# Kernel tuning notes

Measured on AMD Instinct MI355X. Metric: run time of the kernel, lower is better.

Reference implementation:

```python
import jax, jax.numpy as jnp
import numpy as np

DD = 1.5        # delta_d margin from config (paper default)
GAMMA = 0.001   # regularization weight from config (paper default)
K = 32          # number of instance ids (fixed num_segments; labels in [0, K))


def _per_image_loss(feats, labels):
    """feats: (D, H, W) float, labels: (H, W) int. Returns scalar loss."""
    D = feats.shape[0]
    f = feats.reshape(D, -1).T              # (N, D) pixel embeddings
    lab = labels.reshape(-1)                # (N,)

    counts = jax.ops.segment_sum(jnp.ones(lab.shape, f.dtype), lab, num_segments=K)  # (K,)
    present = counts > 0
    safe_cnt = jnp.maximum(counts, 1.0)

    sums = jax.ops.segment_sum(f, lab, num_segments=K)      # (K, D)
    means = sums / safe_cnt[:, None]                        # (K, D)

    # variance term: sum_i ||f_i - mu_{lab_i}||^2, per-instance-normalized
    d2 = jnp.sum((f - means[lab]) ** 2, axis=1)             # (N,)
    var_per = jax.ops.segment_sum(d2, lab, num_segments=K) / safe_cnt
    var_loss = jnp.sum(jnp.where(present, var_per, 0.0))

    # pairwise distance (hinge) term over i < j, only present clusters
    diff = means[:, None, :] - means[None, :, :]            # (K, K, D)
    dsq = jnp.sum(diff ** 2, axis=-1)                       # (K, K)
    pair_mask = jnp.triu(jnp.ones((K, K), bool), 1) & present[:, None] & present[None, :]
    dist = jnp.sqrt(jnp.where(pair_mask, dsq, 1.0))
    hinge = jnp.where(pair_mask & (dist < 2.0 * DD), (2.0 * DD - dist) ** 2, 0.0)
    n_clusters = jnp.sum(present).astype(f.dtype)
    dist_loss = jnp.sum(hinge) / jnp.maximum(n_clusters - 1.0, 1.0)

    # regularization: sum of L2 norms of present means
    m2 = jnp.sum(means ** 2, axis=1)
    reg_loss = jnp.sum(jnp.where(present, jnp.sqrt(jnp.where(present, m2, 1.0)), 0.0))

    return (var_loss + dist_loss + GAMMA * reg_loss) / n_clusters


def setup_inputs() -> dict:
    key = jax.random.key(0)
    k1, k2 = jax.random.split(key)
    B, D, H, W = 4, 64, 512, 512
    features_batch = jax.random.normal(k1, (B, D, H, W), dtype=jnp.float32)
    labels_batch = jax.random.randint(k2, (B, H, W), 0, K, dtype=jnp.int32)
    return {"features_batch": features_batch, "labels_batch": labels_batch}


def reference(features_batch, labels_batch):
    per_image = jax.vmap(_per_image_loss)(features_batch, labels_batch)  # (B,)
    B = features_batch.shape[0]
    return (jnp.sum(per_image) / (B + 1)).reshape(1)
```

## Files before the change

### kernel.cpp

```cpp
#include <hip/hip_runtime.h>
#include <hip/hip_bf16.h>
#include <math.h>


#define KSEG 32
#define DF   64
#define STATS_STRIDE 2112
#define GPB  512

typedef _Float16 half8 __attribute__((ext_vector_type(8)));
typedef float f32x4 __attribute__((ext_vector_type(4)));

__global__ __launch_bounds__(256) void stats_kernel(
    const float* __restrict__ feats, const int* __restrict__ labels,
    float* __restrict__ st, int N) {
  const int b = blockIdx.y, g = blockIdx.x;
  const int tid = threadIdx.x;
  const int w = tid >> 6, lane = tid & 63;
  const int m = lane & 15, q = lane >> 4;

  const float* __restrict__ fimg = feats + (size_t)b * DF * N;
  const int* __restrict__ limg = labels + (size_t)b * N;
  const int pix0 = g * (N / GPB);
  const int d = 16 * w + m;
  const float* __restrict__ frow = fimg + (size_t)d * N;

  f32x4 c_sum0 = {0.f, 0.f, 0.f, 0.f}, c_sum1 = {0.f, 0.f, 0.f, 0.f};
  f32x4 c_sq0 = {0.f, 0.f, 0.f, 0.f}, c_sq1 = {0.f, 0.f, 0.f, 0.f};
  f32x4 c_cn0 = {0.f, 0.f, 0.f, 0.f}, c_cn1 = {0.f, 0.f, 0.f, 0.f};
  const _Float16 h1 = (_Float16)1.0f, h0 = (_Float16)0.0f;
  half8 ones = {h1, h1, h1, h1, h1, h1, h1, h1};

#pragma unroll 4
  for (int c = 0; c < 16; ++c) {
    const int pb = pix0 + c * 32 + q * 8;
    const float4 fA = *(const float4*)(frow + pb);
    const float4 fB = *(const float4*)(frow + pb + 4);
    const int4 lA = *(const int4*)(limg + pb);
    const int4 lB = *(const int4*)(limg + pb + 4);

    float fv[8] = {fA.x, fA.y, fA.z, fA.w, fB.x, fB.y, fB.z, fB.w};
    int lv[8] = {lA.x, lA.y, lA.z, lA.w, lB.x, lB.y, lB.z, lB.w};

    half8 bf, bsq, a0, a1;
#pragma unroll
    for (int j = 0; j < 8; ++j) {
      const _Float16 h = (_Float16)fv[j];
      bf[j] = h;
      bsq[j] = h * h;
      a0[j] = (lv[j] == m) ? h1 : h0;
      a1[j] = (lv[j] == m + 16) ? h1 : h0;
    }
    c_sum0 = __builtin_amdgcn_mfma_f32_16x16x32_f16(a0, bf, c_sum0, 0, 0, 0);
    c_sum1 = __builtin_amdgcn_mfma_f32_16x16x32_f16(a1, bf, c_sum1, 0, 0, 0);
    c_sq0 = __builtin_amdgcn_mfma_f32_16x16x32_f16(a0, bsq, c_sq0, 0, 0, 0);
    c_sq1 = __builtin_amdgcn_mfma_f32_16x16x32_f16(a1, bsq, c_sq1, 0, 0, 0);
    c_cn0 = __builtin_amdgcn_mfma_f32_16x16x32_f16(a0, ones, c_cn0, 0, 0, 0);
    c_cn1 = __builtin_amdgcn_mfma_f32_16x16x32_f16(a1, ones, c_cn1, 0, 0, 0);
  }

  __shared__ float lsum[KSEG][DF + 1];
  __shared__ float lssq[KSEG][DF + 1];
  __shared__ float lcnt[KSEG];
#pragma unroll
  for (int r = 0; r < 4; ++r) {
    const int k0 = q * 4 + r;
    lsum[k0][16 * w + m] = c_sum0[r];
    lsum[k0 + 16][16 * w + m] = c_sum1[r];
    lssq[k0][16 * w + m] = c_sq0[r];
    lssq[k0 + 16][16 * w + m] = c_sq1[r];
  }
  if (w == 0 && m == 0) {
#pragma unroll
    for (int r = 0; r < 4; ++r) {
      lcnt[q * 4 + r] = c_cn0[r];
      lcnt[16 + q * 4 + r] = c_cn1[r];
    }
  }
  __syncthreads();

  float* so = st + (size_t)b * STATS_STRIDE;
  for (int i = tid; i < KSEG * DF; i += 256)
    atomicAdd(&so[i], lsum[i >> 6][i & 63]);
  if (tid < KSEG) {
    float s = 0.f;
    for (int dd = 0; dd < DF; ++dd) s += lssq[tid][dd];
    atomicAdd(&so[KSEG * DF + tid], lcnt[tid]);
    atomicAdd(&so[KSEG * DF + KSEG + tid], s);
  }
}

__global__ __launch_bounds__(256) void finalize_kernel(
    const float* __restrict__ st, float* __restrict__ out, int B) {
  __shared__ float mu[KSEG][DF + 1];
  __shared__ float cntS[KSEG], ssqS[KSEG], musqS[KSEG];
  __shared__ float wred[4];
  const int tid = threadIdx.x;
  float total = 0.f;

  for (int b = 0; b < B; ++b) {
    const float* base = st + (size_t)b * STATS_STRIDE;
    if (tid < KSEG) {
      cntS[tid] = base[KSEG * DF + tid];
      ssqS[tid] = base[KSEG * DF + KSEG + tid];
    }
    __syncthreads();
    for (int idx = tid; idx < KSEG * DF; idx += 256) {
      const int k = idx >> 6, dd = idx & 63;
      mu[k][dd] = base[idx] / fmaxf(cntS[k], 1.f);
    }
    __syncthreads();
    if (tid < KSEG) {
      float m2 = 0.f;
      for (int dd = 0; dd < DF; ++dd) m2 = fmaf(mu[tid][dd], mu[tid][dd], m2);
      musqS[tid] = m2;
    }
    __syncthreads();

    float hacc = 0.f;
    for (int p = tid; p < KSEG * KSEG; p += 256) {
      const int i = p >> 5, j = p & 31;
      if (i < j && cntS[i] > 0.f && cntS[j] > 0.f) {
        float dsq = 0.f;
        for (int dd = 0; dd < DF; ++dd) {
          const float df = mu[i][dd] - mu[j][dd];
          dsq = fmaf(df, df, dsq);
        }
        const float h = 2.f * 1.5f - sqrtf(dsq);
        if (h > 0.f) hacc += h * h;
      }
    }
    for (int off = 32; off > 0; off >>= 1) hacc += __shfl_down(hacc, off, 64);
    if ((tid & 63) == 0) wred[tid >> 6] = hacc;
    __syncthreads();

    if (tid == 0) {
      const float dsum = wred[0] + wred[1] + wred[2] + wred[3];
      float var = 0.f, reg = 0.f, ncl = 0.f;
      for (int k = 0; k < KSEG; ++k) {
        const float c = cntS[k];
        if (c > 0.f) {
          ncl += 1.f;
          var += ssqS[k] / c - musqS[k];
          reg += sqrtf(musqS[k]);
        }
      }
      const float dist_loss = dsum / fmaxf(ncl - 1.f, 1.f);
      total += (var + dist_loss + 0.001f * reg) / ncl;
    }
    __syncthreads();
  }
  if (tid == 0) out[0] = total / (float)(B + 1);
}

extern "C" void kernel_launch(void* const* d_in, const int* in_sizes, int n_in,
                              void* d_out, int out_size, void* d_ws, size_t ws_size,
                              hipStream_t stream) {
  const float* feats = (const float*)d_in[0];
  const int* labels = (const int*)d_in[1];
  float* out = (float*)d_out;

  const int B = 4;
  const int BHW = in_sizes[1];
  const int N = BHW / B;

  float* st = (float*)d_ws;
  hipMemsetAsync(st, 0, (size_t)B * STATS_STRIDE * sizeof(float), stream);

  stats_kernel<<<dim3(GPB, B), 256, 0, stream>>>(feats, labels, st, N);
  finalize_kernel<<<1, 256, 0, stream>>>(st, out, B);
}
```

Measured before the change: 419.8 us.

## Replace global atomics with per-block partials and a two-stage tree reduction

Each stats block now writes its per-segment partial sums to its own workspace slot instead of atomically adding into one shared buffer per image. A new reduce kernel sums the partials in 16 groups, and finalize runs one block per image, adding its loss into the output with an atomic. This removes heavy atomic contention (about 2K atomics from each of 2048 blocks onto the same addresses) and the memset, at the cost of roughly 17 MB of extra partial traffic and an extra kernel launch. Zeroing the output inside reduce_kernel relies on stream ordering before finalize.

After: 398.9 us. 5.0% less time.

```diff
diff --git a/kernel.cpp b/kernel.cpp
--- a/kernel.cpp
+++ b/kernel.cpp
@@ -1,5 +1,4 @@
 #include <hip/hip_runtime.h>
-#include <hip/hip_bf16.h>
 #include <math.h>
 
 
@@ -7,13 +6,15 @@
 #define DF   64
 #define STATS_STRIDE 2112
 #define GPB  512
+#define ZSPLIT 16
+#define GPZ  (GPB / ZSPLIT)
 
 typedef _Float16 half8 __attribute__((ext_vector_type(8)));
 typedef float f32x4 __attribute__((ext_vector_type(4)));
 
 __global__ __launch_bounds__(256) void stats_kernel(
     const float* __restrict__ feats, const int* __restrict__ labels,
-    float* __restrict__ st, int N) {
+    float* __restrict__ partial, int N) {
   const int b = blockIdx.y, g = blockIdx.x;
   const int tid = threadIdx.x;
   const int w = tid >> 6, lane = tid & 63;
@@ -79,78 +80,97 @@
   }
   __syncthreads();
 
-  float* so = st + (size_t)b * STATS_STRIDE;
+  float* so = partial + (size_t)(b * GPB + g) * STATS_STRIDE;
   for (int i = tid; i < KSEG * DF; i += 256)
-    atomicAdd(&so[i], lsum[i >> 6][i & 63]);
+    so[i] = lsum[i >> 6][i & 63];
   if (tid < KSEG) {
     float s = 0.f;
     for (int dd = 0; dd < DF; ++dd) s += lssq[tid][dd];
-    atomicAdd(&so[KSEG * DF + tid], lcnt[tid]);
-    atomicAdd(&so[KSEG * DF + KSEG + tid], s);
+    so[KSEG * DF + tid] = lcnt[tid];
+    so[KSEG * DF + KSEG + tid] = s;
   }
 }
 
+__global__ __launch_bounds__(256) void reduce_kernel(
+    const float* __restrict__ partial, float* __restrict__ p2,
+    float* __restrict__ out) {
+  if (blockIdx.x == 0 && blockIdx.y == 0 && blockIdx.z == 0 && threadIdx.x == 0)
+    out[0] = 0.f;
+  const int idx = blockIdx.x * 256 + threadIdx.x;
+  if (idx >= STATS_STRIDE) return;
+  const int b = blockIdx.y, z = blockIdx.z;
+  const float* __restrict__ src =
+      partial + (size_t)(b * GPB + z * GPZ) * STATS_STRIDE + idx;
+  float s = 0.f;
+#pragma unroll 8
+  for (int g = 0; g < GPZ; ++g) s += src[(size_t)g * STATS_STRIDE];
+  p2[(size_t)(b * ZSPLIT + z) * STATS_STRIDE + idx] = s;
+}
+
 __global__ __launch_bounds__(256) void finalize_kernel(
-    const float* __restrict__ st, float* __restrict__ out, int B) {
+    const float* __restrict__ p2, float* __restrict__ out) {
   __shared__ float mu[KSEG][DF + 1];
   __shared__ float cntS[KSEG], ssqS[KSEG], musqS[KSEG];
   __shared__ float wred[4];
   const int tid = threadIdx.x;
-  float total = 0.f;
+  const int b = blockIdx.x;
+  const float* __restrict__ base = p2 + (size_t)b * ZSPLIT * STATS_STRIDE;
 
-  for (int b = 0; b < B; ++b) {
-    const float* base = st + (size_t)b * STATS_STRIDE;
-    if (tid < KSEG) {
-      cntS[tid] = base[KSEG * DF + tid];
-      ssqS[tid] = base[KSEG * DF + KSEG + tid];
+  if (tid < KSEG) {
+    float c = 0.f, s = 0.f;
+    for (int z = 0; z < ZSPLIT; ++z) {
+      c += base[(size_t)z * STATS_STRIDE + KSEG * DF + tid];
+      s += base[(size_t)z * STATS_STRIDE + KSEG * DF + KSEG + tid];
     }
-    __syncthreads();
-    for (int idx = tid; idx < KSEG * DF; idx += 256) {
-      const int k = idx >> 6, dd = idx & 63;
-      mu[k][dd] = base[idx] / fmaxf(cntS[k], 1.f);
+    cntS[tid] = c;
+    ssqS[tid] = s;
+  }
+  __syncthreads();
+  for (int idx = tid; idx < KSEG * DF; idx += 256) {
+    float s = 0.f;
+    for (int z = 0; z < ZSPLIT; ++z) s += base[(size_t)z * STATS_STRIDE + idx];
+    mu[idx >> 6][idx & 63] = s / fmaxf(cntS[idx >> 6], 1.f);
+  }
+  __syncthreads();
+  if (tid < KSEG) {
+    float m2 = 0.f;
+    for (int dd = 0; dd < DF; ++dd) m2 = fmaf(mu[tid][dd], mu[tid][dd], m2);
+    musqS[tid] = m2;
+  }
+  __syncthreads();
+
+  float hacc = 0.f;
+  for (int p = tid; p < KSEG * KSEG; p += 256) {
+    const int i = p >> 5, j = p & 31;
+    if (i < j && cntS[i] > 0.f && cntS[j] > 0.f) {
+      float dsq = 0.f;
+      for (int dd = 0; dd < DF; ++dd) {
+        const float df = mu[i][dd] - mu[j][dd];
+        dsq = fmaf(df, df, dsq);
+      }
+      const float h = 2.f * 1.5f - sqrtf(dsq);
+      if (h > 0.f) hacc += h * h;
     }
-    __syncthreads();
-    if (tid < KSEG) {
-      float m2 = 0.f;
-      for (int dd = 0; dd < DF; ++dd) m2 = fmaf(mu[tid][dd], mu[tid][dd], m2);
-      musqS[tid] = m2;
-    }
-    __syncthreads();
+  }
+  for (int off = 32; off > 0; off >>= 1) hacc += __shfl_down(hacc, off, 64);
+  if ((tid & 63) == 0) wred[tid >> 6] = hacc;
+  __syncthreads();
 
-    float hacc = 0.f;
-    for (int p = tid; p < KSEG * KSEG; p += 256) {
-      const int i = p >> 5, j = p & 31;
-      if (i < j && cntS[i] > 0.f && cntS[j] > 0.f) {
-        float dsq = 0.f;
-        for (int dd = 0; dd < DF; ++dd) {
-          const float df = mu[i][dd] - mu[j][dd];
-          dsq = fmaf(df, df, dsq);
-        }
-        const float h = 2.f * 1.5f - sqrtf(dsq);
-        if (h > 0.f) hacc += h * h;
+  if (tid == 0) {
+    const float dsum = wred[0] + wred[1] + wred[2] + wred[3];
+    float var = 0.f, reg = 0.f, ncl = 0.f;
+    for (int k = 0; k < KSEG; ++k) {
+      const float c = cntS[k];
+      if (c > 0.f) {
+        ncl += 1.f;
+        var += ssqS[k] / c - musqS[k];
+        reg += sqrtf(musqS[k]);
       }
     }
-    for (int off = 32; off > 0; off >>= 1) hacc += __shfl_down(hacc, off, 64);
-    if ((tid & 63) == 0) wred[tid >> 6] = hacc;
-    __syncthreads();
-
-    if (tid == 0) {
-      const float dsum = wred[0] + wred[1] + wred[2] + wred[3];
-      float var = 0.f, reg = 0.f, ncl = 0.f;
-      for (int k = 0; k < KSEG; ++k) {
-        const float c = cntS[k];
-        if (c > 0.f) {
-          ncl += 1.f;
-          var += ssqS[k] / c - musqS[k];
-          reg += sqrtf(musqS[k]);
-        }
-      }
-      const float dist_loss = dsum / fmaxf(ncl - 1.f, 1.f);
-      total += (var + dist_loss + 0.001f * reg) / ncl;
-    }
-    __syncthreads();
+    const float dist_loss = dsum / fmaxf(ncl - 1.f, 1.f);
+    const float loss = (var + dist_loss + 0.001f * reg) / ncl;
+    atomicAdd(out, loss / (float)(gridDim.x + 1));
   }
-  if (tid == 0) out[0] = total / (float)(B + 1);
 }
 
 extern "C" void kernel_launch(void* const* d_in, const int* in_sizes, int n_in,
@@ -164,9 +184,11 @@
   const int BHW = in_sizes[1];
   const int N = BHW / B;
 
-  float* st = (float*)d_ws;
-  hipMemsetAsync(st, 0, (size_t)B * STATS_STRIDE * sizeof(float), stream);
+  float* partial = (float*)d_ws;
+  float* p2 = partial + (size_t)B * GPB * STATS_STRIDE;
 
-  stats_kernel<<<dim3(GPB, B), 256, 0, stream>>>(feats, labels, st, N);
-  finalize_kernel<<<1, 256, 0, stream>>>(st, out, B);
+  stats_kernel<<<dim3(GPB, B), 256, 0, stream>>>(feats, labels, partial, N);
+  reduce_kernel<<<dim3((STATS_STRIDE + 255) / 256, B, ZSPLIT), 256, 0, stream>>>(
+      partial, p2, out);
+  finalize_kernel<<<dim3(B), 256, 0, stream>>>(p2, out);
 }
```
